# Kernel optimization log

Measured on AMD Instinct MI355X. Metric: run time of the kernel, lower is better.

The kernel has to match this reference:

```python
import jax, jax.numpy as jnp
import numpy as np

B, T, C = 2, 2048, 1024
HS, DS = 8, 32      # short heads, short qk dim
HL, DL = 8, 128     # long heads, long qk dim
HD = 64             # value/output head dim = n_embd // n_head
WIN_S, WIN_L = 256, 1024
NEG = jnp.finfo(jnp.float32).min


def _window_mask(t, window):
    # additive mask: disallow future (i<j) and tokens older than the window
    i = jnp.arange(t)[:, None]
    j = jnp.arange(t)[None, :]
    bad = (i - j < 0) | (i - j >= window)
    return bad.astype(jnp.float32) * NEG  # [T,T]


def _attn(x, Wqk, Wv, n_h, d_qk, d_v, window):
    b, t, _ = x.shape
    qk = x @ Wqk                                      # [B,T,2*n_h*d_qk]
    q, k = jnp.split(qk, 2, axis=-1)
    q = q.reshape(b, t, n_h, d_qk).transpose(0, 2, 1, 3)  # [B,H,T,dqk]
    k = k.reshape(b, t, n_h, d_qk).transpose(0, 2, 1, 3)
    v = (x @ Wv).reshape(b, t, n_h, d_v).transpose(0, 2, 1, 3)  # [B,H,T,dv]
    scale = 1.0 / jnp.sqrt(jnp.float32(d_qk))
    scores = jnp.einsum('bhqd,bhkd->bhqk', q, k) * scale
    scores = scores + _window_mask(t, window)
    p = jax.nn.softmax(scores, axis=-1)
    return jnp.einsum('bhqk,bhkd->bhqd', p, v)        # [B,H,T,dv]


def setup_inputs() -> dict:
    key = jax.random.key(0)
    ks = jax.random.split(key, 6)
    s = 0.02
    return {
        'x': jax.random.normal(ks[0], (B, T, C), dtype=jnp.float32),
        'Wqk_short': jax.random.normal(ks[1], (C, 2 * HS * DS), dtype=jnp.float32) * s,
        'Wv_short': jax.random.normal(ks[2], (C, HS * HD), dtype=jnp.float32) * s,
        'Wqk_long': jax.random.normal(ks[3], (C, 2 * HL * DL), dtype=jnp.float32) * s,
        'Wv_long': jax.random.normal(ks[4], (C, HL * HD), dtype=jnp.float32) * s,
        'Wproj': jax.random.normal(ks[5], (C, C), dtype=jnp.float32) * s,
    }


def reference(x, Wqk_short, Wv_short, Wqk_long, Wv_long, Wproj):
    b, t, c = x.shape
    y_short = _attn(x, Wqk_short, Wv_short, HS, DS, HD, WIN_S)  # [B,HS,T,HD]
    y_long = _attn(x, Wqk_long, Wv_long, HL, DL, HD, WIN_L)     # [B,HL,T,HD]
    y = jnp.concatenate([y_short, y_long], axis=1)              # [B,H,T,HD]
    y = y.transpose(0, 2, 1, 3).reshape(b, t, c)
    return y @ Wproj
```

## Files before the change

### kernel.cpp

```cpp
#include <hip/hip_runtime.h>
#include <math.h>

#define B_    2
#define T_    2048
#define C_    1024
#define HS_   8
#define DS_   32
#define HL_   8
#define DL_   128
#define HD_   64
#define WINS_ 256
#define WINL_ 1024
#define NALL_ 3584

typedef __bf16 bf16x8 __attribute__((ext_vector_type(8)));
typedef float floatx4 __attribute__((ext_vector_type(4)));

__device__ __forceinline__ ushort f2bf(float f) {
    union { float f; unsigned u; } v; v.f = f;
    unsigned r = v.u + 0x7fff + ((v.u >> 16) & 1);
    return (ushort)(r >> 16);
}
__device__ __forceinline__ float bf2f(ushort u) {
    union { unsigned u; float f; } v; v.u = ((unsigned)u) << 16;
    return v.f;
}

#define DPP_STEP(x, ctrl, op)                                                \
    {                                                                        \
        float _t = __builtin_bit_cast(                                       \
            float, __builtin_amdgcn_update_dpp(                              \
                       0, __builtin_bit_cast(int, (x)), (ctrl), 0xf, 0xf,    \
                       true));                                               \
        (x) = op((x), _t);                                                   \
    }
__device__ __forceinline__ float dpp_max16(float x) {
    DPP_STEP(x, 0xB1, fmaxf);
    DPP_STEP(x, 0x4E, fmaxf);
    DPP_STEP(x, 0x141, fmaxf);
    DPP_STEP(x, 0x140, fmaxf);
    return x;
}
__device__ __forceinline__ float dpp_add16(float x) {
#define FADD_(a, b) ((a) + (b))
    DPP_STEP(x, 0xB1, FADD_);
    DPP_STEP(x, 0x4E, FADD_);
    DPP_STEP(x, 0x141, FADD_);
    DPP_STEP(x, 0x140, FADD_);
#undef FADD_
    return x;
}

__device__ __forceinline__ void gload_lds16(const void* g, void* l) {
    __builtin_amdgcn_global_load_lds(
        (const __attribute__((address_space(1))) void*)g,
        (__attribute__((address_space(3))) void*)l, 16, 0, 0);
}

__global__ __launch_bounds__(256) void prep(
    const float* __restrict__ x, ushort* __restrict__ x16,
    const float* __restrict__ Wqk_s, const float* __restrict__ Wv_s,
    const float* __restrict__ Wqk_l, const float* __restrict__ Wv_l,
    const float* __restrict__ Wproj, ushort* __restrict__ WallT,
    ushort* __restrict__ WprojT) {
    __shared__ float t[32][33];
    int bid = blockIdx.x;
    if (bid < 4096) {
        const int i = bid * 256 + threadIdx.x;
        float4 v = ((const float4*)x)[i];
        ushort4 o;
        o.x = f2bf(v.x); o.y = f2bf(v.y); o.z = f2bf(v.z); o.w = f2bf(v.w);
        ((ushort4*)x16)[i] = o;
        return;
    }
    bid -= 4096;
    const float* W; ushort* WT; int N, rowoff;
    if (bid < 512)       { W = Wqk_s; WT = WallT;  N = 512;  rowoff = 0; }
    else if (bid < 1024) { bid -= 512;  W = Wv_s;  WT = WallT;  N = 512;  rowoff = 512; }
    else if (bid < 3072) { bid -= 1024; W = Wqk_l; WT = WallT;  N = 2048; rowoff = 1024; }
    else if (bid < 3584) { bid -= 3072; W = Wv_l;  WT = WallT;  N = 512;  rowoff = 3072; }
    else                 { bid -= 3584; W = Wproj; WT = WprojT; N = 1024; rowoff = 0; }
    const int nt = N / 32;
    const int n0 = (bid % nt) * 32;
    const int k0 = (bid / nt) * 32;
    const int tx = threadIdx.x & 31;
    const int ty = threadIdx.x >> 5;
#pragma unroll
    for (int i = 0; i < 4; ++i)
        t[ty + 8 * i][tx] = W[(size_t)(k0 + ty + 8 * i) * N + n0 + tx];
    __syncthreads();
#pragma unroll
    for (int i = 0; i < 4; ++i)
        WT[(size_t)(rowoff + n0 + ty + 8 * i) * 1024 + k0 + tx] =
            f2bf(t[tx][ty + 8 * i]);
}

template <int BM, typename OT, bool FUSEV>
__global__ __launch_bounds__(256) void gemm_bf16(const ushort* __restrict__ A,
                                                 const ushort* __restrict__ BT,
                                                 OT* __restrict__ Cm,
                                                 ushort* __restrict__ VT,
                                                 int M, int N, int K) {
    __shared__ ushort As[2][BM * 32];
    __shared__ ushort Bs[2][128 * 32];
    constexpr int NI = BM / 32;
    const int tid = threadIdx.x;
    const int m0 = blockIdx.y * BM;
    const int n0 = blockIdx.x * 128;
    const int wave = tid >> 6;
    const int lane = tid & 63;
    const int wm = (wave >> 1) * (BM / 2);
    const int wn = (wave & 1) * 64;
    const int l15 = lane & 15;
    const int quad = lane >> 4;

    const int srow = tid >> 2;
    const int sc = (tid & 3) * 8;

    floatx4 acc[NI][4] = {};

    const ushort* Ap0 = A + (size_t)(m0 + srow) * K + sc;
    const ushort* Ap1 = A + (size_t)(m0 + (srow & 63) + 64) * K + sc;
    const ushort* Bp0 = BT + (size_t)(n0 + srow) * K + sc;
    const ushort* Bp1 = BT + (size_t)(n0 + srow + 64) * K + sc;

    const int aoff0 = wave * 512;
    const int aoff1 = (wave * 512 + 2048) % (BM * 32);
    const int boff0 = wave * 512;
    const int boff1 = wave * 512 + 2048;

#define STAGE(buf, kt)                                                \
    {                                                                 \
        gload_lds16(Ap0 + (kt), &As[buf][aoff0]);                     \
        if constexpr (BM == 128) gload_lds16(Ap1 + (kt), &As[buf][aoff1]); \
        gload_lds16(Bp0 + (kt), &Bs[buf][boff0]);                     \
        gload_lds16(Bp1 + (kt), &Bs[buf][boff1]);                     \
    }

#define COMPUTE(buf)                                                       \
    {                                                                      \
        bf16x8 af[NI], bfr[4];                                             \
        _Pragma("unroll") for (int i = 0; i < NI; ++i) af[i] =             \
            *(const bf16x8*)&As[buf][(wm + i * 16 + l15) * 32 + quad * 8]; \
        _Pragma("unroll") for (int j = 0; j < 4; ++j) bfr[j] =             \
            *(const bf16x8*)&Bs[buf][(wn + j * 16 + l15) * 32 + quad * 8]; \
        _Pragma("unroll") for (int i = 0; i < NI; ++i)                     \
            _Pragma("unroll") for (int j = 0; j < 4; ++j) acc[i][j] =      \
                __builtin_amdgcn_mfma_f32_16x16x32_bf16(af[i], bfr[j],     \
                                                        acc[i][j], 0, 0, 0); \
    }

    STAGE(0, 0);
    __syncthreads();
    for (int kt = 0; kt < K; kt += 64) {
        STAGE(1, kt + 32);
        COMPUTE(0);
        __syncthreads();
        if (kt + 64 < K) STAGE(0, kt + 64);
        COMPUTE(1);
        __syncthreads();
    }
#undef STAGE
#undef COMPUTE

    bool vtile = false;
    if constexpr (FUSEV)
        vtile = (n0 >= 512 && n0 < 1024) || (n0 >= 3072);

    if (FUSEV && vtile) {
#pragma unroll
        for (int i = 0; i < NI; ++i) {
            const int m = m0 + wm + i * 16 + quad * 4;
            const int bb = m >> 11;
            const int t = m & 2047;
#pragma unroll
            for (int j = 0; j < 4; ++j) {
                const int col = n0 + wn + j * 16 + l15;
                const int vcol = (col < 1024) ? (col - 512) : (col - 2560);
                ushort4 val;
                val.x = f2bf(acc[i][j][0]);
                val.y = f2bf(acc[i][j][1]);
                val.z = f2bf(acc[i][j][2]);
                val.w = f2bf(acc[i][j][3]);
                *(ushort4*)&VT[((size_t)(bb * 1024 + vcol)) * T_ + t] = val;
            }
        }
    } else {
#pragma unroll
        for (int i = 0; i < NI; ++i)
#pragma unroll
            for (int j = 0; j < 4; ++j)
#pragma unroll
                for (int r = 0; r < 4; ++r) {
                    const size_t idx =
                        (size_t)(m0 + wm + i * 16 + quad * 4 + r) * N + n0 +
                        wn + j * 16 + l15;
                    if constexpr (sizeof(OT) == 2)
                        Cm[idx] = f2bf(acc[i][j][r]);
                    else
                        Cm[idx] = acc[i][j][r];
                }
    }
}

template <int D, int WIN, bool SPLIT>
__device__ __forceinline__ void attn_dev(
    const ushort* __restrict__ act, const ushort* __restrict__ vt,
    ushort* __restrict__ y, ushort* __restrict__ po, float* __restrict__ pm,
    float* __restrict__ pl, float scale2, int qoff, int koff, int head_off,
    int h, int gh, int b, int t0, int zs, ushort* lds) {
    constexpr int STR = D + 8;
    constexpr int PSTR = 72;
    constexpr int NKS = D / 32;
    constexpr int QCH = D / 8;
    constexpr int NKLD = (64 * QCH) / 256;

    ushort* Ks = lds;
    ushort* VTs = Ks + 64 * STR;
    ushort* Ps = VTs + 64 * PSTR;

    const int tid = threadIdx.x;
    const int wave = tid >> 6;
    const int lane = tid & 63;
    const int l15 = lane & 15;
    const int quad = lane >> 4;
    const int qmin = t0 + wave * 16;

    int k0s = t0 - WIN + 1;
    if (k0s < 0) k0s = 0;
    k0s &= ~63;

    int ks_begin = k0s, ks_last = t0;
    if (SPLIT) {
        const int nt = ((t0 - k0s) >> 6) + 1;
        const int ntlo = (nt + 1) >> 1;
        if (zs == 0) {
            ks_last = k0s + (ntlo - 1) * 64;
        } else {
            if (ntlo >= nt) {
#pragma unroll
                for (int r = 0; r < 4; ++r) {
                    const int t = qmin + quad * 4 + r;
                    const size_t ridx =
                        (((size_t)(zs * 2 + b) * 8 + h) * T_ + t);
                    if (l15 == 0) { pm[ridx] = -1e30f; pl[ridx] = 0.f; }
#pragma unroll
                    for (int j = 0; j < 4; ++j)
                        po[ridx * 64 + j * 16 + l15] = 0;
                }
                return;
            }
            ks_begin = k0s + ntlo * 64;
        }
    }

    const ushort* qbase = act + (size_t)(b * T_ + t0) * NALL_ + qoff + h * D;
    const ushort* kbase = act + (size_t)(b * T_) * NALL_ + koff + h * D;
    const ushort* vtb = vt + (size_t)((b * 16 + gh) * HD_) * T_;

    int krow[NKLD], kch[NKLD];
#pragma unroll
    for (int i = 0; i < NKLD; ++i) {
        const int idx = tid + 256 * i;
        krow[i] = idx / QCH;
        kch[i] = idx % QCH;
    }
    const int vd0 = tid >> 3, vc0 = (tid & 7) * 8;
    const int vd1 = (tid + 256) >> 3, vc1 = ((tid + 256) & 7) * 8;

    int4 kreg[NKLD], vreg0, vreg1;
#pragma unroll
    for (int i = 0; i < NKLD; ++i)
        kreg[i] = *(const int4*)(kbase + (size_t)(ks_begin + krow[i]) * NALL_ +
                                 kch[i] * 8);
    vreg0 = *(const int4*)(vtb + (size_t)vd0 * T_ + ks_begin + vc0);
    vreg1 = *(const int4*)(vtb + (size_t)vd1 * T_ + ks_begin + vc1);

    for (int idx = tid; idx < 64 * QCH; idx += 256) {
        const int row = idx / QCH;
        const int ch = idx % QCH;
        *(int4*)&Ks[row * STR + ch * 8] =
            *(const int4*)(qbase + (size_t)row * NALL_ + ch * 8);
    }
    __syncthreads();
    bf16x8 qa[NKS];
#pragma unroll
    for (int ks = 0; ks < NKS; ++ks)
        qa[ks] = *(const bf16x8*)&Ks[(wave * 16 + l15) * STR + ks * 32 + quad * 8];

    float m_i[4], l_i[4];
    floatx4 o_acc[4] = {};
#pragma unroll
    for (int r = 0; r < 4; ++r) { m_i[r] = -1e30f; l_i[r] = 0.f; }

    for (int k0 = ks_begin; k0 <= ks_last; k0 += 64) {
        __syncthreads();
#pragma unroll
        for (int i = 0; i < NKLD; ++i)
            *(int4*)&Ks[krow[i] * STR + kch[i] * 8] = kreg[i];
        *(int4*)&VTs[vd0 * PSTR + vc0] = vreg0;
        *(int4*)&VTs[vd1 * PSTR + vc1] = vreg1;
        __syncthreads();
        if (k0 + 64 <= ks_last) {
#pragma unroll
            for (int i = 0; i < NKLD; ++i)
                kreg[i] = *(const int4*)(kbase +
                                         (size_t)(k0 + 64 + krow[i]) * NALL_ +
                                         kch[i] * 8);
            vreg0 = *(const int4*)(vtb + (size_t)vd0 * T_ + k0 + 64 + vc0);
            vreg1 = *(const int4*)(vtb + (size_t)vd1 * T_ + k0 + 64 + vc1);
        }

        floatx4 s[4] = {};
#pragma unroll
        for (int ks = 0; ks < NKS; ++ks) {
#pragma unroll
            for (int j = 0; j < 4; ++j) {
                const bf16x8 bb =
                    *(const bf16x8*)&Ks[(j * 16 + l15) * STR + ks * 32 + quad * 8];
                s[j] = __builtin_amdgcn_mfma_f32_16x16x32_bf16(qa[ks], bb, s[j],
                                                               0, 0, 0);
            }
        }

        const bool full = (k0 + 63 <= qmin) && ((qmin + 15) - k0 <= WIN - 1);
        if (full) {
#pragma unroll
            for (int j = 0; j < 4; ++j)
#pragma unroll
                for (int r = 0; r < 4; ++r) s[j][r] *= scale2;
        } else {
#pragma unroll
            for (int j = 0; j < 4; ++j) {
                const int kj = k0 + j * 16 + l15;
#pragma unroll
                for (int r = 0; r < 4; ++r) {
                    const int rel = (qmin + quad * 4 + r) - kj;
                    s[j][r] = (rel < 0 || rel >= WIN) ? -1e30f : s[j][r] * scale2;
                }
            }
        }

#pragma unroll
        for (int r = 0; r < 4; ++r) {
            float rm = fmaxf(fmaxf(s[0][r], s[1][r]), fmaxf(s[2][r], s[3][r]));
            rm = dpp_max16(rm);
            const float mn = fmaxf(m_i[r], rm);
            const float a = exp2f(m_i[r] - mn);
            m_i[r] = mn;
            float sum = 0.f;
#pragma unroll
            for (int j = 0; j < 4; ++j) {
                const float e = exp2f(s[j][r] - mn);
                sum += e;
                Ps[(wave * 16 + quad * 4 + r) * PSTR + j * 16 + l15] = f2bf(e);
            }
            sum = dpp_add16(sum);
            l_i[r] = l_i[r] * a + sum;
#pragma unroll
            for (int j = 0; j < 4; ++j) o_acc[j][r] *= a;
        }

#pragma unroll
        for (int kks = 0; kks < 2; ++kks) {
            const bf16x8 pa =
                *(const bf16x8*)&Ps[(wave * 16 + l15) * PSTR + kks * 32 + quad * 8];
#pragma unroll
            for (int j = 0; j < 4; ++j) {
                const bf16x8 vb =
                    *(const bf16x8*)&VTs[(j * 16 + l15) * PSTR + kks * 32 + quad * 8];
                o_acc[j] = __builtin_amdgcn_mfma_f32_16x16x32_bf16(pa, vb, o_acc[j],
                                                                   0, 0, 0);
            }
        }
    }

    if (SPLIT) {
#pragma unroll
        for (int r = 0; r < 4; ++r) {
            const int t = qmin + quad * 4 + r;
            const size_t ridx = (((size_t)(zs * 2 + b) * 8 + h) * T_ + t);
            if (l15 == 0) { pm[ridx] = m_i[r]; pl[ridx] = l_i[r]; }
#pragma unroll
            for (int j = 0; j < 4; ++j)
                po[ridx * 64 + j * 16 + l15] = f2bf(o_acc[j][r]);
        }
    } else {
#pragma unroll
        for (int r = 0; r < 4; ++r) {
            const float inv = 1.f / l_i[r];
            ushort* yrow = y + (size_t)(b * T_ + qmin + quad * 4 + r) * C_ +
                           head_off + h * HD_;
#pragma unroll
            for (int j = 0; j < 4; ++j)
                yrow[j * 16 + l15] = f2bf(o_acc[j][r] * inv);
        }
    }
}

__global__ __launch_bounds__(256, 4) void attn_sched(
    const ushort* __restrict__ act, const ushort* __restrict__ vt,
    ushort* __restrict__ y, ushort* __restrict__ po, float* __restrict__ pm,
    float* __restrict__ pl) {
    extern __shared__ ushort smem[];
    int x = blockIdx.x;
    if (x < 1024) {
        const int zs = x & 1;
        const int b = (x >> 1) & 1;
        const int h = (x >> 2) & 7;
        const int t0 = (31 - (x >> 5)) * 64;
        attn_dev<DL_, WINL_, true>(act, vt, y, po, pm, pl,
                                   0.12752021352994164f,
                                   1024, 2048, 512, h, 8 + h, b, t0, zs, smem);
    } else {
        x -= 1024;
        const int b = x & 1;
        const int h = (x >> 1) & 7;
        const int t0 = (31 - (x >> 4)) * 64;
        attn_dev<DS_, WINS_, false>(act, vt, y, po, pm, pl,
                                    0.2550404270598833f,
                                    0, 256, 0, h, h, b, t0, 0, smem);
    }
}

__global__ __launch_bounds__(256) void combine(const ushort* __restrict__ po,
                                               const float* __restrict__ pm,
                                               const float* __restrict__ pl,
                                               ushort* __restrict__ y) {
    const int gid = blockIdx.x * 256 + threadIdx.x;
    const int row = gid >> 4;
    const int cg = (gid & 15) * 4;
    const int b = row >> 14;
    const int h = (row >> 11) & 7;
    const int t = row & 2047;

    const float m0 = pm[row], m1 = pm[32768 + row];
    const float l0 = pl[row], l1 = pl[32768 + row];
    const float m = fmaxf(m0, m1);
    const float e0 = exp2f(m0 - m);
    const float e1 = exp2f(m1 - m);
    const float inv = 1.f / (l0 * e0 + l1 * e1);

    const ushort4 o0 = *(const ushort4*)&po[(size_t)row * 64 + cg];
    const ushort4 o1 = *(const ushort4*)&po[((size_t)32768 + row) * 64 + cg];

    ushort4 r;
    r.x = f2bf((bf2f(o0.x) * e0 + bf2f(o1.x) * e1) * inv);
    r.y = f2bf((bf2f(o0.y) * e0 + bf2f(o1.y) * e1) * inv);
    r.z = f2bf((bf2f(o0.z) * e0 + bf2f(o1.z) * e1) * inv);
    r.w = f2bf((bf2f(o0.w) * e0 + bf2f(o1.w) * e1) * inv);
    *(ushort4*)&y[(size_t)(b * T_ + t) * C_ + 512 + h * 64 + cg] = r;
}

extern "C" void kernel_launch(void* const* d_in, const int* in_sizes, int n_in,
                              void* d_out, int out_size, void* d_ws,
                              size_t ws_size, hipStream_t stream) {
    const float* x         = (const float*)d_in[0];
    const float* Wqk_short = (const float*)d_in[1];
    const float* Wv_short  = (const float*)d_in[2];
    const float* Wqk_long  = (const float*)d_in[3];
    const float* Wv_long   = (const float*)d_in[4];
    const float* Wproj     = (const float*)d_in[5];
    float* out = (float*)d_out;

    const int M = B_ * T_;

    ushort* x16    = (ushort*)d_ws;
    ushort* WallT  = x16 + (size_t)M * C_;
    ushort* WprojT = WallT + (size_t)NALL_ * C_;
    ushort* yb16   = WprojT + (size_t)C_ * C_;
    ushort* act    = yb16 + (size_t)M * C_;
    ushort* vt     = act + (size_t)M * NALL_;
    ushort* po     = vt + (size_t)32 * HD_ * T_;
    float*  pm     = (float*)(po + (size_t)2 * 32768 * 64);
    float*  pl     = pm + (size_t)2 * 32768;

    dim3 blk(256);
    prep<<<dim3(8704), blk, 0, stream>>>(x, x16, Wqk_short, Wv_short, Wqk_long,
                                         Wv_long, Wproj, WallT, WprojT);

    gemm_bf16<128, ushort, true><<<dim3(NALL_ / 128, M / 128), blk, 0, stream>>>(
        x16, WallT, act, vt, M, NALL_, C_);

    const int attn_lds = (64 * (DL_ + 8) + 64 * 72 * 2) * 2;
    attn_sched<<<dim3(1536), blk, attn_lds, stream>>>(act, vt, yb16, po, pm, pl);

    combine<<<dim3(2048), blk, 0, stream>>>(po, pm, pl, yb16);

    gemm_bf16<64, float, false><<<dim3(C_ / 128, M / 64), blk, 0, stream>>>(
        yb16, WprojT, out, nullptr, M, C_, C_);
}
```

Measured before the change: 219.7 us.

## Triple-buffer GEMM LDS tiles with vmcnt waits and one barrier per step

Switches the bf16 GEMM main loop from double buffering with two __syncthreads per 64-wide K step to a three-slot ring advancing 32 K per iteration. Each step waits with an explicit s_waitcnt vmcnt on only the current tile's async global-to-LDS loads, then issues a single barrier. This keeps two tiles of loads in flight while computing and halves the barrier count. In exchange, LDS use grows by half, which may lower occupancy, and correctness now depends on the hand-counted vmcnt values.

```diff
diff --git a/kernel.cpp b/kernel.cpp
--- a/kernel.cpp
+++ b/kernel.cpp
@@ -101,8 +101,8 @@
                                                  OT* __restrict__ Cm,
                                                  ushort* __restrict__ VT,
                                                  int M, int N, int K) {
-    __shared__ ushort As[2][BM * 32];
-    __shared__ ushort Bs[2][128 * 32];
+    __shared__ ushort As[3][BM * 32];
+    __shared__ ushort Bs[3][128 * 32];
     constexpr int NI = BM / 32;
     const int tid = threadIdx.x;
     const int m0 = blockIdx.y * BM;
@@ -129,12 +129,12 @@
     const int boff0 = wave * 512;
     const int boff1 = wave * 512 + 2048;
 
-#define STAGE(buf, kt)                                                \
-    {                                                                 \
-        gload_lds16(Ap0 + (kt), &As[buf][aoff0]);                     \
+#define STAGE(buf, kt)                                                     \
+    {                                                                      \
+        gload_lds16(Ap0 + (kt), &As[buf][aoff0]);                          \
         if constexpr (BM == 128) gload_lds16(Ap1 + (kt), &As[buf][aoff1]); \
-        gload_lds16(Bp0 + (kt), &Bs[buf][boff0]);                     \
-        gload_lds16(Bp1 + (kt), &Bs[buf][boff1]);                     \
+        gload_lds16(Bp0 + (kt), &Bs[buf][boff0]);                          \
+        gload_lds16(Bp1 + (kt), &Bs[buf][boff1]);                          \
     }
 
 #define COMPUTE(buf)                                                       \
@@ -150,18 +150,37 @@
                                                         acc[i][j], 0, 0, 0); \
     }
 
+#define WAIT_CUR()                                                    \
+    {                                                                 \
+        if constexpr (BM == 128)                                      \
+            asm volatile("s_waitcnt vmcnt(4)" ::: "memory");          \
+        else                                                          \
+            asm volatile("s_waitcnt vmcnt(3)" ::: "memory");          \
+    }
+
     STAGE(0, 0);
-    __syncthreads();
-    for (int kt = 0; kt < K; kt += 64) {
-        STAGE(1, kt + 32);
-        COMPUTE(0);
-        __syncthreads();
-        if (kt + 64 < K) STAGE(0, kt + 64);
-        COMPUTE(1);
-        __syncthreads();
-    }
+    STAGE(1, 32);
+    int cur = 0;
+    for (int kt = 0; kt + 32 < K; kt += 32) {
+        WAIT_CUR();
+        __builtin_amdgcn_s_barrier();
+        __builtin_amdgcn_sched_barrier(0);
+        if (kt + 64 < K) {
+            int nxt2 = cur + 2;
+            if (nxt2 >= 3) nxt2 -= 3;
+            STAGE(nxt2, kt + 64);
+        }
+        COMPUTE(cur);
+        ++cur;
+        if (cur == 3) cur = 0;
+    }
+    asm volatile("s_waitcnt vmcnt(0)" ::: "memory");
+    __builtin_amdgcn_s_barrier();
+    __builtin_amdgcn_sched_barrier(0);
+    COMPUTE(cur);
 #undef STAGE
 #undef COMPUTE
+#undef WAIT_CUR
 
     bool vtile = false;
     if constexpr (FUSEV)
```

Measured after the change: 214.7 us. 2.3% less time.
